# Kernel tuning notes

Hardware: AMD Instinct MI355X
Metric: run time of the kernel (lower is better)

## Reference

```python
import jax, jax.numpy as jnp
import numpy as np

N_IN = 512
SCALE = 0  # s / n_in**scale == s when scale=0

def setup_inputs() -> dict:
    key = jax.random.key(0)
    k1, k2, k3, k4 = jax.random.split(key, 4)
    B, S, D = 4, 128, N_IN
    x = jax.random.normal(k1, (B, S, D), dtype=jnp.float32)
    y = jax.random.normal(k2, (B, S, D), dtype=jnp.float32)
    z = jax.random.normal(k3, (B, S, D), dtype=jnp.float32)
    # weight: (n_out, n_in + bias_x, n_in, n_in + bias_y)
    weight = jax.random.normal(k4, (1, D + 1, D, D + 1), dtype=jnp.float32) * 0.02
    return {"x": x, "y": y, "z": z, "weight": weight}

def reference(x, y, z, weight):
    # append bias-1 column to x and y (bias_x=bias_y=True)
    ones = jnp.ones_like(x[..., :1])
    xb = jnp.concatenate([x, ones], axis=-1)           # [b, s, n_in+1]
    yb = jnp.concatenate([y, jnp.ones_like(y[..., :1])], axis=-1)
    # w = z^T W : [b, o, z, i, j]
    w = jnp.einsum('bzk,oikj->bozij', z, weight)
    # s(x,y,z) = x^T (z^T W) y : [b, o, z, x, y]
    s = jnp.einsum('bxi,bozij,byj->bozxy', xb, w, yb)
    # n_out == 1 -> squeeze channel dim; scale == 0 -> divide by n_in**0 == 1
    return jnp.squeeze(s, axis=1) / (N_IN ** SCALE)
```

## Files before the change

### kernel.cpp

```cpp
#include <hip/hip_runtime.h>
#include <stdint.h>


typedef __attribute__((ext_vector_type(8))) short bf16x8;
typedef __attribute__((ext_vector_type(4))) float f32x4;

__device__ __forceinline__ unsigned short f2bf(float f) {
    unsigned int u = __float_as_uint(f);
    u += 0x7fffu + ((u >> 16) & 1u);
    return (unsigned short)(u >> 16);
}

__device__ __forceinline__ void gload_lds16(const void* g, void* l) {
    __builtin_amdgcn_global_load_lds((const __attribute__((address_space(1))) void*)g,
                                     (__attribute__((address_space(3))) void*)l, 16, 0, 0);
}

__global__ __launch_bounds__(256) void k_cast(const float* __restrict__ x,
    const float* __restrict__ y, const float* __restrict__ z,
    unsigned short* __restrict__ xbf, unsigned short* __restrict__ ybf,
    unsigned short* __restrict__ zbf)
{
    int t = blockIdx.x * 256 + threadIdx.x;
    int arr = t >> 15;
    int off = (t & 32767) * 8;
    const float* src = (arr == 0) ? x : (arr == 1) ? y : z;
    unsigned short* dst = (arr == 0) ? xbf : (arr == 1) ? ybf : zbf;
    float4 a = *(const float4*)(src + off);
    float4 b = *(const float4*)(src + off + 4);
    uint4 o;
    o.x = f2bf(a.x) | ((unsigned)f2bf(a.y) << 16);
    o.y = f2bf(a.z) | ((unsigned)f2bf(a.w) << 16);
    o.z = f2bf(b.x) | ((unsigned)f2bf(b.y) << 16);
    o.w = f2bf(b.z) | ((unsigned)f2bf(b.w) << 16);
    *(uint4*)(dst + off) = o;
}

__global__ __launch_bounds__(256) void k_edge(const float* __restrict__ z,
    const float* __restrict__ w, float* __restrict__ a_arr,
    float* __restrict__ c_arr, float* __restrict__ d_arr)
{
    __shared__ float Zs[64][33];
    __shared__ float Bs[32][65];
    int t = threadIdx.x;
    int mb = blockIdx.x % 17, bzb = blockIdx.x / 17;
    int tr = t >> 4, tc = t & 15;
    float acc[4][4] = {};
    for (int k0 = 0; k0 < 512; k0 += 32) {
        __syncthreads();
        {   int row = t >> 2, ko = (t & 3) * 8;
            const float* p = z + (bzb * 64 + row) * 512 + k0 + ko;
            float4 v0 = ((const float4*)p)[0], v1 = ((const float4*)p)[1];
            Zs[row][ko + 0] = v0.x; Zs[row][ko + 1] = v0.y; Zs[row][ko + 2] = v0.z; Zs[row][ko + 3] = v0.w;
            Zs[row][ko + 4] = v1.x; Zs[row][ko + 5] = v1.y; Zs[row][ko + 6] = v1.z; Zs[row][ko + 7] = v1.w;
        }
        {   int kr = t >> 3, mo = (t & 7) * 8;
            for (int e = 0; e < 8; ++e) {
                int m = mb * 64 + mo + e;
                float v = 0.f;
                int krow = k0 + kr;
                if (m < 512)        v = w[(m * 512 + krow) * 513 + 512];
                else if (m < 1024)  v = w[(262144 + krow) * 513 + (m - 512)];
                else if (m == 1024) v = w[(262144 + krow) * 513 + 512];
                Bs[kr][mo + e] = v;
            }
        }
        __syncthreads();
        for (int kk = 0; kk < 32; ++kk) {
            float zr[4], br[4];
            for (int r = 0; r < 4; ++r) zr[r] = Zs[tr * 4 + r][kk];
            for (int c = 0; c < 4; ++c) br[c] = Bs[kk][tc * 4 + c];
            for (int r = 0; r < 4; ++r)
                for (int c = 0; c < 4; ++c) acc[r][c] += zr[r] * br[c];
        }
    }
    for (int r = 0; r < 4; ++r)
        for (int c = 0; c < 4; ++c) {
            int bz = bzb * 64 + tr * 4 + r;
            int m = mb * 64 + tc * 4 + c;
            if (m < 512)        a_arr[bz * 512 + m] = acc[r][c];
            else if (m < 1024)  c_arr[bz * 512 + (m - 512)] = acc[r][c];
            else if (m == 1024) d_arr[bz] = acc[r][c];
        }
}

__global__ __launch_bounds__(512) void k_uv(const float* __restrict__ xf,
    const float* __restrict__ yf, const float* __restrict__ a_arr,
    const float* __restrict__ c_arr, float* __restrict__ u_arr,
    float* __restrict__ v_arr)
{
    __shared__ float part[512];
    int bz = blockIdx.x;
    int b = bz >> 7;
    int t = threadIdx.x, r = t >> 2, q = t & 3;
    {
        const float* xp = xf + (size_t)(b * 128 + r) * 512;
        const float* ap = a_arr + bz * 512;
        float s = 0.f;
        #pragma unroll 4
        for (int c0 = 0; c0 < 32; ++c0) {
            int col = c0 * 16 + q * 4;
            float4 xv = *(const float4*)(xp + col);
            float4 av = *(const float4*)(ap + col);
            s += xv.x * av.x + xv.y * av.y + xv.z * av.z + xv.w * av.w;
        }
        part[t] = s;
    }
    __syncthreads();
    if (t < 128) u_arr[bz * 128 + t] = part[t*4] + part[t*4+1] + part[t*4+2] + part[t*4+3];
    __syncthreads();
    {
        const float* yp = yf + (size_t)(b * 128 + r) * 512;
        const float* cp = c_arr + bz * 512;
        float s = 0.f;
        #pragma unroll 4
        for (int c0 = 0; c0 < 32; ++c0) {
            int col = c0 * 16 + q * 4;
            float4 yv = *(const float4*)(yp + col);
            float4 cv = *(const float4*)(cp + col);
            s += yv.x * cv.x + yv.y * cv.y + yv.z * cv.z + yv.w * cv.w;
        }
        part[t] = s;
    }
    __syncthreads();
    if (t < 128) v_arr[bz * 128 + t] = part[t*4] + part[t*4+1] + part[t*4+2] + part[t*4+3];
}

__global__ __launch_bounds__(512, 2) void k_gemm1(const unsigned short* __restrict__ zbf,
    const float* __restrict__ w, unsigned short* __restrict__ Mws)
{
    extern __shared__ unsigned char smem[];
    unsigned char* Zb0 = smem;
    unsigned char* Zb1 = smem + 32768;
    unsigned char* Bb0 = smem + 65536;
    unsigned char* Bb1 = smem + 73728;

    int nwg = gridDim.x, cpx = nwg >> 3;
    int bid = blockIdx.x;
    int swz = (bid & 7) * cpx + (bid >> 3);
    int iloc = swz >> 2, jb = swz & 3;
    int j0 = jb * 128;
    int t = threadIdx.x, wid = t >> 6, lane = t & 63;
    int bzg = wid >> 1, jg = wid & 1;
    int l15 = lane & 15, l4 = lane >> 4;

    int arow = lane >> 2;
    int akc  = (lane & 3) ^ ((lane >> 3) & 3);
    const unsigned short* zbase = zbf + (size_t)(wid * 64 + arow) * 512 + akc * 8;

    int jB = t & 127, kq8 = t >> 7;
    const float* wb = w + (size_t)iloc * 262656 + (size_t)(kq8 * 8) * 513 + j0 + jB;
    int bwoff = jB * 64 + ((kq8 ^ ((jB >> 1) & 3)) * 16);

    int aoff = (bzg * 128 + l15) * 64 + ((l4 ^ ((l15 >> 1) & 3)) * 16);
    int boff = (jg * 64 + l15) * 64 + ((l4 ^ ((l15 >> 1) & 3)) * 16);

    f32x4 acc[8][4];
    #pragma unroll
    for (int mt = 0; mt < 8; ++mt)
        #pragma unroll
        for (int nt = 0; nt < 4; ++nt) acc[mt][nt] = (f32x4){0.f, 0.f, 0.f, 0.f};

    float wr[2][8];

    #pragma unroll
    for (int q = 0; q < 4; ++q)
        gload_lds16(zbase + q * 8192, Zb0 + wid * 4096 + q * 1024);
    {
        #pragma unroll
        for (int e = 0; e < 8; ++e) wr[0][e] = __builtin_nontemporal_load(wb + (size_t)e * 513);
        const float* wp = wb + (size_t)32 * 513;
        #pragma unroll
        for (int e = 0; e < 8; ++e) wr[1][e] = __builtin_nontemporal_load(wp + (size_t)e * 513);
        uint4 pk;
        pk.x = f2bf(wr[0][0]) | ((unsigned)f2bf(wr[0][1]) << 16);
        pk.y = f2bf(wr[0][2]) | ((unsigned)f2bf(wr[0][3]) << 16);
        pk.z = f2bf(wr[0][4]) | ((unsigned)f2bf(wr[0][5]) << 16);
        pk.w = f2bf(wr[0][6]) | ((unsigned)f2bf(wr[0][7]) << 16);
        *(uint4*)(Bb0 + bwoff) = pk;
    }
    asm volatile("s_waitcnt lgkmcnt(0)" ::: "memory");
    __builtin_amdgcn_s_barrier();
    __builtin_amdgcn_sched_barrier(0);

    #pragma unroll
    for (int ks = 0; ks < 16; ++ks) {
        const int cur = ks & 1;
        unsigned char* Zcur  = cur ? Zb1 : Zb0;
        unsigned char* Znext = cur ? Zb0 : Zb1;
        unsigned char* Bcur  = cur ? Bb1 : Bb0;
        unsigned char* Bnext = cur ? Bb0 : Bb1;

        if (ks < 15) {
            #pragma unroll
            for (int q = 0; q < 4; ++q)
                gload_lds16(zbase + (ks + 1) * 32 + q * 8192, Znext + wid * 4096 + q * 1024);
        }
        if (ks < 14) {
            const float* wp = wb + (size_t)(ks + 2) * 32 * 513;
            #pragma unroll
            for (int e = 0; e < 8; ++e) wr[cur][e] = __builtin_nontemporal_load(wp + (size_t)e * 513);
        }
        bf16x8 bfr[4];
        #pragma unroll
        for (int nt = 0; nt < 4; ++nt)
            bfr[nt] = *(const bf16x8*)(Bcur + boff + nt * 1024);
        #pragma unroll
        for (int mt = 0; mt < 8; ++mt) {
            bf16x8 afr = *(const bf16x8*)(Zcur + aoff + mt * 1024);
            #pragma unroll
            for (int nt = 0; nt < 4; ++nt)
                acc[mt][nt] = __builtin_amdgcn_mfma_f32_16x16x32_bf16(afr, bfr[nt], acc[mt][nt], 0, 0, 0);
        }
        if (ks < 15) {
            uint4 pk;
            pk.x = f2bf(wr[cur ^ 1][0]) | ((unsigned)f2bf(wr[cur ^ 1][1]) << 16);
            pk.y = f2bf(wr[cur ^ 1][2]) | ((unsigned)f2bf(wr[cur ^ 1][3]) << 16);
            pk.z = f2bf(wr[cur ^ 1][4]) | ((unsigned)f2bf(wr[cur ^ 1][5]) << 16);
            pk.w = f2bf(wr[cur ^ 1][6]) | ((unsigned)f2bf(wr[cur ^ 1][7]) << 16);
            *(uint4*)(Bnext + bwoff) = pk;
        }
        if (ks < 14) {
            asm volatile("s_waitcnt vmcnt(8) lgkmcnt(0)" ::: "memory");
        } else if (ks == 14) {
            asm volatile("s_waitcnt vmcnt(0) lgkmcnt(0)" ::: "memory");
        }
        if (ks < 15) {
            __builtin_amdgcn_s_barrier();
            __builtin_amdgcn_sched_barrier(0);
        }
    }

    #pragma unroll
    for (int mt = 0; mt < 8; ++mt)
        #pragma unroll
        for (int nt = 0; nt < 4; ++nt)
            #pragma unroll
            for (int r = 0; r < 4; ++r) {
                int bz = bzg * 128 + mt * 16 + l4 * 4 + r;
                int j  = j0 + jg * 64 + nt * 16 + l15;
                Mws[(size_t)bz * 262144 + (size_t)iloc * 512 + j] = f2bf(acc[mt][nt][r]);
            }
}

__global__ __launch_bounds__(512, 2) void k_fuse(const unsigned short* __restrict__ xbf,
    const unsigned short* __restrict__ ybf, const unsigned short* __restrict__ Mws,
    const float* __restrict__ u_arr, const float* __restrict__ v_arr,
    const float* __restrict__ d_arr, float* __restrict__ out)
{
    extern __shared__ unsigned char smem[];

    int bid = blockIdx.x;
    int bz = (bid & 7) * 64 + (bid >> 3);
    int b = bz >> 7;
    int t = threadIdx.x, wid = t >> 6, lane = t & 63;
    int l15 = lane & 15, l4 = lane >> 4;
    int xg = wid >> 2, yg = wid & 3;
    int g8 = wid;

    const unsigned short* ybase = ybf + (size_t)(b * 128) * 512;
    #pragma unroll
    for (int it = 0; it < 16; ++it) {
        int row = it * 8 + wid;
        gload_lds16(ybase + (size_t)row * 512 + ((lane ^ (row & 63)) * 8),
                    smem + it * 8192 + t * 16);
    }

    const unsigned short* mbase = Mws + (size_t)bz * 262144
                                + (size_t)(g8 * 64 + l15) * 512 + l4 * 8;
    bf16x8 mfr[4][4];
    #pragma unroll
    for (int d = 0; d < 4; ++d)
        #pragma unroll
        for (int mt = 0; mt < 4; ++mt)
            mfr[d][mt] = *(const bf16x8*)(mbase + (size_t)mt * 8192 + d * 32);

    asm volatile("s_waitcnt vmcnt(16)" ::: "memory");
    __builtin_amdgcn_s_barrier();
    __builtin_amdgcn_sched_barrier(0);

    f32x4 accR[4][8];
    #pragma unroll
    for (int mt = 0; mt < 4; ++mt)
        #pragma unroll
        for (int nt = 0; nt < 8; ++nt) accR[mt][nt] = (f32x4){0.f, 0.f, 0.f, 0.f};

    #pragma unroll
    for (int kf = 0; kf < 16; ++kf) {
        #pragma unroll
        for (int nh = 0; nh < 2; ++nh) {
            bf16x8 yfr[4];
            #pragma unroll
            for (int n4 = 0; n4 < 4; ++n4) {
                int y = (nh * 4 + n4) * 16 + l15;
                yfr[n4] = *(const bf16x8*)(smem + y * 1024 + (((kf * 4 + l4) ^ (y & 63)) * 16));
            }
            #pragma unroll
            for (int mt = 0; mt < 4; ++mt)
                #pragma unroll
                for (int n4 = 0; n4 < 4; ++n4)
                    accR[mt][nh * 4 + n4] = __builtin_amdgcn_mfma_f32_16x16x32_bf16(
                        mfr[kf & 3][mt], yfr[n4], accR[mt][nh * 4 + n4], 0, 0, 0);
        }
        if (kf < 12) {
            #pragma unroll
            for (int mt = 0; mt < 4; ++mt)
                mfr[kf & 3][mt] = *(const bf16x8*)(mbase + (size_t)mt * 8192 + (kf + 4) * 32);
        }
    }

    const unsigned short* xbase = xbf + (size_t)(b * 128 + xg * 64 + l15) * 512 + l4 * 8;
    bf16x8 xfr[3][4];
    #pragma unroll
    for (int d = 0; d < 3; ++d)
        #pragma unroll
        for (int mt = 0; mt < 4; ++mt)
            xfr[d][mt] = *(const bf16x8*)(xbase + (size_t)mt * 8192 + d * 32);

    asm volatile("s_waitcnt lgkmcnt(0)" ::: "memory");
    __builtin_amdgcn_s_barrier();
    __builtin_amdgcn_sched_barrier(0);

    #pragma unroll
    for (int mt = 0; mt < 4; ++mt)
        #pragma unroll
        for (int nt = 0; nt < 8; ++nt) {
            int y = nt * 16 + l15;
            int chunk = g8 * 8 + mt * 2 + (l4 >> 1);
            int byte = y * 1024 + ((chunk ^ (y & 63)) * 16) + (l4 & 1) * 8;
            unsigned p0 = f2bf(accR[mt][nt][0]) | ((unsigned)f2bf(accR[mt][nt][1]) << 16);
            unsigned p1 = f2bf(accR[mt][nt][2]) | ((unsigned)f2bf(accR[mt][nt][3]) << 16);
            *(uint2*)(smem + byte) = make_uint2(p0, p1);
        }
    asm volatile("s_waitcnt lgkmcnt(0)" ::: "memory");
    __builtin_amdgcn_s_barrier();
    __builtin_amdgcn_sched_barrier(0);

    f32x4 acc[4][2];
    #pragma unroll
    for (int mt = 0; mt < 4; ++mt)
        #pragma unroll
        for (int nt = 0; nt < 2; ++nt) acc[mt][nt] = (f32x4){0.f, 0.f, 0.f, 0.f};

    #pragma unroll
    for (int kf = 0; kf < 16; ++kf) {
        bf16x8 rfr[2];
        #pragma unroll
        for (int nt = 0; nt < 2; ++nt) {
            int y = yg * 32 + nt * 16 + l15;
            rfr[nt] = *(const bf16x8*)(smem + y * 1024 + (((kf * 4 + l4) ^ (y & 63)) * 16));
        }
        #pragma unroll
        for (int mt = 0; mt < 4; ++mt)
            #pragma unroll
            for (int nt = 0; nt < 2; ++nt)
                acc[mt][nt] = __builtin_amdgcn_mfma_f32_16x16x32_bf16(
                    xfr[kf % 3][mt], rfr[nt], acc[mt][nt], 0, 0, 0);
        if (kf < 13) {
            #pragma unroll
            for (int mt = 0; mt < 4; ++mt)
                xfr[kf % 3][mt] = *(const bf16x8*)(xbase + (size_t)mt * 8192 + (kf + 3) * 32);
        }
    }

    float dv = d_arr[bz];
    float* op = out + (size_t)bz * 16384;
    #pragma unroll
    for (int mt = 0; mt < 4; ++mt) {
        float4 uq = *(const float4*)(u_arr + bz * 128 + xg * 64 + mt * 16 + l4 * 4);
        #pragma unroll
        for (int nt = 0; nt < 2; ++nt) {
            int y = yg * 32 + nt * 16 + l15;
            float vv = v_arr[bz * 128 + y] + dv;
            int x0 = xg * 64 + mt * 16 + l4 * 4;
            op[(x0 + 0) * 128 + y] = acc[mt][nt][0] + uq.x + vv;
            op[(x0 + 1) * 128 + y] = acc[mt][nt][1] + uq.y + vv;
            op[(x0 + 2) * 128 + y] = acc[mt][nt][2] + uq.z + vv;
            op[(x0 + 3) * 128 + y] = acc[mt][nt][3] + uq.w + vv;
        }
    }
}

extern "C" void kernel_launch(void* const* d_in, const int* in_sizes, int n_in,
                              void* d_out, int out_size, void* d_ws, size_t ws_size,
                              hipStream_t stream)
{
    const float* x = (const float*)d_in[0];
    const float* y = (const float*)d_in[1];
    const float* z = (const float*)d_in[2];
    const float* w = (const float*)d_in[3];
    float* out = (float*)d_out;
    char* ws = (char*)d_ws;

    unsigned short* xbf = (unsigned short*)(ws + 0);
    unsigned short* ybf = (unsigned short*)(ws + 524288);
    unsigned short* zbf = (unsigned short*)(ws + 1048576);
    float* a_arr = (float*)(ws + 1572864);
    float* c_arr = (float*)(ws + 2621440);
    float* d_arr = (float*)(ws + 3670016);
    float* u_arr = (float*)(ws + 3674112);
    float* v_arr = (float*)(ws + 3936256);
    unsigned short* Mws = (unsigned short*)(ws + 4198400);

    hipLaunchKernelGGL(k_cast, dim3(384), dim3(256), 0, stream, x, y, z, xbf, ybf, zbf);
    hipLaunchKernelGGL(k_edge, dim3(136), dim3(256), 0, stream, z, w, a_arr, c_arr, d_arr);
    hipLaunchKernelGGL(k_uv, dim3(512), dim3(512), 0, stream, x, y, a_arr, c_arr, u_arr, v_arr);
    hipLaunchKernelGGL(k_gemm1, dim3(2048), dim3(512), 81920, stream, zbf, w, Mws);
    hipLaunchKernelGGL(k_fuse, dim3(512), dim3(512), 131072, stream, xbf, ybf, Mws,
                       u_arr, v_arr, d_arr, out);
}
```

Measured before the change: 445.5 us.

## Retile gemm1 to 256x256 tiles with K=64 stages and phased MFMA schedule

Restructures the z×W GEMM kernel from 512x128 output tiles with K=32 steps to 256x256 tiles with K=64 steps, each split into four barrier-separated MFMA phases. The aim is less per-iteration barrier and fp32-to-bf16 weight-conversion overhead per MFMA, better reuse of each loaded weight column, and overlap of global loads with compute through an interleaved ping-pong schedule and s_setprio. The cost is 128KB of LDS per block, which likely limits each CU to one block, plus more barriers per K-step and plain rather than nontemporal weight loads.

```diff
diff --git a/kernel.cpp b/kernel.cpp
--- a/kernel.cpp
+++ b/kernel.cpp
@@ -130,116 +130,153 @@
     const float* __restrict__ w, unsigned short* __restrict__ Mws)
 {
     extern __shared__ unsigned char smem[];
-    unsigned char* Zb0 = smem;
-    unsigned char* Zb1 = smem + 32768;
-    unsigned char* Bb0 = smem + 65536;
-    unsigned char* Bb1 = smem + 73728;
-
-    int nwg = gridDim.x, cpx = nwg >> 3;
+    unsigned char* const Ab0 = smem;
+    unsigned char* const Ab1 = smem + 32768;
+    unsigned char* const Bb0 = smem + 65536;
+    unsigned char* const Bb1 = smem + 98304;
+
     int bid = blockIdx.x;
-    int swz = (bid & 7) * cpx + (bid >> 3);
-    int iloc = swz >> 2, jb = swz & 3;
-    int j0 = jb * 128;
+    int swz = (bid & 7) * 256 + (bid >> 3);
+    int mt2 = swz & 1;
+    int panel = swz >> 1;
+    int jb = panel & 1, iw = panel >> 1;
+    int bz0 = mt2 * 256;
+    int jlo = jb * 256;
     int t = threadIdx.x, wid = t >> 6, lane = t & 63;
-    int bzg = wid >> 1, jg = wid & 1;
+    int wm = wid >> 2, wn = wid & 3;
     int l15 = lane & 15, l4 = lane >> 4;
 
-    int arow = lane >> 2;
-    int akc  = (lane & 3) ^ ((lane >> 3) & 3);
-    const unsigned short* zbase = zbf + (size_t)(wid * 64 + arow) * 512 + akc * 8;
-
-    int jB = t & 127, kq8 = t >> 7;
-    const float* wb = w + (size_t)iloc * 262656 + (size_t)(kq8 * 8) * 513 + j0 + jB;
-    int bwoff = jB * 64 + ((kq8 ^ ((jB >> 1) & 3)) * 16);
-
-    int aoff = (bzg * 128 + l15) * 64 + ((l4 ^ ((l15 >> 1) & 3)) * 16);
-    int boff = (jg * 64 + l15) * 64 + ((l4 ^ ((l15 >> 1) & 3)) * 16);
+    int ar = t >> 3;
+    int ac = (t & 7) ^ (ar & 7);
+    const unsigned short* zsrc = zbf + (size_t)(bz0 + ar) * 512 + ac * 8;
+
+    int jB = t & 127, s2 = t >> 7;
+    const float* wsrc = w + (size_t)iw * 262656 + (size_t)(s2 * 16) * 513 + jlo + jB;
+    int bw0 = jB * 128 + (((s2 * 2)     ^ (jB & 7)) * 16);
+    int bw1 = jB * 128 + (((s2 * 2 + 1) ^ (jB & 7)) * 16);
+
+    int axr = l15 & 7;
+    int abase = (wm * 128 + l15) * 128;
+    int bbase = (wn * 64 + l15) * 128;
 
     f32x4 acc[8][4];
     #pragma unroll
-    for (int mt = 0; mt < 8; ++mt)
-        #pragma unroll
-        for (int nt = 0; nt < 4; ++nt) acc[mt][nt] = (f32x4){0.f, 0.f, 0.f, 0.f};
-
-    float wr[2][8];
-
-    #pragma unroll
-    for (int q = 0; q < 4; ++q)
-        gload_lds16(zbase + q * 8192, Zb0 + wid * 4096 + q * 1024);
-    {
-        #pragma unroll
-        for (int e = 0; e < 8; ++e) wr[0][e] = __builtin_nontemporal_load(wb + (size_t)e * 513);
-        const float* wp = wb + (size_t)32 * 513;
-        #pragma unroll
-        for (int e = 0; e < 8; ++e) wr[1][e] = __builtin_nontemporal_load(wp + (size_t)e * 513);
-        uint4 pk;
-        pk.x = f2bf(wr[0][0]) | ((unsigned)f2bf(wr[0][1]) << 16);
-        pk.y = f2bf(wr[0][2]) | ((unsigned)f2bf(wr[0][3]) << 16);
-        pk.z = f2bf(wr[0][4]) | ((unsigned)f2bf(wr[0][5]) << 16);
-        pk.w = f2bf(wr[0][6]) | ((unsigned)f2bf(wr[0][7]) << 16);
-        *(uint4*)(Bb0 + bwoff) = pk;
-    }
-    asm volatile("s_waitcnt lgkmcnt(0)" ::: "memory");
+    for (int f = 0; f < 8; ++f)
+        #pragma unroll
+        for (int g = 0; g < 4; ++g) acc[f][g] = (f32x4){0.f, 0.f, 0.f, 0.f};
+
+    float wr0[16], wr1[16];
+    bf16x8 af[4][2], bfA[2][2], bfB[2][2];
+
+#define LDW(dst, kt, h) { const float* _p = wsrc + (size_t)(kt) * 64 * 513 + (h) * 128; \
+    _Pragma("unroll") for (int _e = 0; _e < 16; ++_e) dst[_e] = _p[(size_t)_e * 513]; }
+
+#define STAGE_A(buf, kt) { int _ko = (kt) * 64; \
+    gload_lds16(zsrc + _ko,          (buf) + t * 16); \
+    gload_lds16(zsrc + 32768 + _ko,  (buf) + 8192 + t * 16); \
+    gload_lds16(zsrc + 65536 + _ko,  (buf) + 16384 + t * 16); \
+    gload_lds16(zsrc + 98304 + _ko,  (buf) + 24576 + t * 16); }
+
+#define PACKW(buf, half, src) { uint4 _pa, _pb; \
+    _pa.x = f2bf(src[0])  | ((unsigned)f2bf(src[1])  << 16); \
+    _pa.y = f2bf(src[2])  | ((unsigned)f2bf(src[3])  << 16); \
+    _pa.z = f2bf(src[4])  | ((unsigned)f2bf(src[5])  << 16); \
+    _pa.w = f2bf(src[6])  | ((unsigned)f2bf(src[7])  << 16); \
+    _pb.x = f2bf(src[8])  | ((unsigned)f2bf(src[9])  << 16); \
+    _pb.y = f2bf(src[10]) | ((unsigned)f2bf(src[11]) << 16); \
+    _pb.z = f2bf(src[12]) | ((unsigned)f2bf(src[13]) << 16); \
+    _pb.w = f2bf(src[14]) | ((unsigned)f2bf(src[15]) << 16); \
+    *(uint4*)((buf) + (half) * 16384 + bw0) = _pa; \
+    *(uint4*)((buf) + (half) * 16384 + bw1) = _pb; }
+
+#define LD_A(buf, mq) { _Pragma("unroll") for (int _f = 0; _f < 4; ++_f) \
+    _Pragma("unroll") for (int _kc = 0; _kc < 2; ++_kc) \
+    af[_f][_kc] = *(const bf16x8*)((buf) + abase + ((mq) * 64 + _f * 16) * 128 \
+                                   + (((_kc * 4 + l4) ^ axr) * 16)); }
+
+#define LD_B(buf, nq, dst) { _Pragma("unroll") for (int _g = 0; _g < 2; ++_g) \
+    _Pragma("unroll") for (int _kc = 0; _kc < 2; ++_kc) \
+    dst[_g][_kc] = *(const bf16x8*)((buf) + bbase + ((nq) * 32 + _g * 16) * 128 \
+                                    + (((_kc * 4 + l4) ^ axr) * 16)); }
+
+#define MM(mq, nq, bfr) { _Pragma("unroll") for (int _f = 0; _f < 4; ++_f) \
+    _Pragma("unroll") for (int _g = 0; _g < 2; ++_g) \
+    _Pragma("unroll") for (int _kc = 0; _kc < 2; ++_kc) \
+    acc[(mq) * 4 + _f][(nq) * 2 + _g] = __builtin_amdgcn_mfma_f32_16x16x32_bf16( \
+        af[_f][_kc], bfr[_g][_kc], acc[(mq) * 4 + _f][(nq) * 2 + _g], 0, 0, 0); }
+
+#define PH_SYNC() { __builtin_amdgcn_s_barrier(); \
+    asm volatile("s_waitcnt lgkmcnt(0)" ::: "memory"); \
+    __builtin_amdgcn_sched_barrier(0); }
+#define PH_END() { __builtin_amdgcn_s_barrier(); __builtin_amdgcn_sched_barrier(0); }
+
+    LDW(wr0, 0, 0);
+    LDW(wr1, 0, 1);
+    STAGE_A(Ab0, 0);
+    PACKW(Bb0, 0, wr0);
+    PACKW(Bb0, 1, wr1);
+    asm volatile("s_waitcnt vmcnt(0) lgkmcnt(0)" ::: "memory");
     __builtin_amdgcn_s_barrier();
     __builtin_amdgcn_sched_barrier(0);
 
     #pragma unroll
-    for (int ks = 0; ks < 16; ++ks) {
-        const int cur = ks & 1;
-        unsigned char* Zcur  = cur ? Zb1 : Zb0;
-        unsigned char* Znext = cur ? Zb0 : Zb1;
-        unsigned char* Bcur  = cur ? Bb1 : Bb0;
-        unsigned char* Bnext = cur ? Bb0 : Bb1;
-
-        if (ks < 15) {
-            #pragma unroll
-            for (int q = 0; q < 4; ++q)
-                gload_lds16(zbase + (ks + 1) * 32 + q * 8192, Znext + wid * 4096 + q * 1024);
-        }
-        if (ks < 14) {
-            const float* wp = wb + (size_t)(ks + 2) * 32 * 513;
-            #pragma unroll
-            for (int e = 0; e < 8; ++e) wr[cur][e] = __builtin_nontemporal_load(wp + (size_t)e * 513);
-        }
-        bf16x8 bfr[4];
-        #pragma unroll
-        for (int nt = 0; nt < 4; ++nt)
-            bfr[nt] = *(const bf16x8*)(Bcur + boff + nt * 1024);
-        #pragma unroll
-        for (int mt = 0; mt < 8; ++mt) {
-            bf16x8 afr = *(const bf16x8*)(Zcur + aoff + mt * 1024);
-            #pragma unroll
-            for (int nt = 0; nt < 4; ++nt)
-                acc[mt][nt] = __builtin_amdgcn_mfma_f32_16x16x32_bf16(afr, bfr[nt], acc[mt][nt], 0, 0, 0);
-        }
-        if (ks < 15) {
-            uint4 pk;
-            pk.x = f2bf(wr[cur ^ 1][0]) | ((unsigned)f2bf(wr[cur ^ 1][1]) << 16);
-            pk.y = f2bf(wr[cur ^ 1][2]) | ((unsigned)f2bf(wr[cur ^ 1][3]) << 16);
-            pk.z = f2bf(wr[cur ^ 1][4]) | ((unsigned)f2bf(wr[cur ^ 1][5]) << 16);
-            pk.w = f2bf(wr[cur ^ 1][6]) | ((unsigned)f2bf(wr[cur ^ 1][7]) << 16);
-            *(uint4*)(Bnext + bwoff) = pk;
-        }
-        if (ks < 14) {
-            asm volatile("s_waitcnt vmcnt(8) lgkmcnt(0)" ::: "memory");
-        } else if (ks == 14) {
-            asm volatile("s_waitcnt vmcnt(0) lgkmcnt(0)" ::: "memory");
-        }
-        if (ks < 15) {
-            __builtin_amdgcn_s_barrier();
-            __builtin_amdgcn_sched_barrier(0);
-        }
-    }
-
-    #pragma unroll
-    for (int mt = 0; mt < 8; ++mt)
-        #pragma unroll
-        for (int nt = 0; nt < 4; ++nt)
+    for (int kt = 0; kt < 8; ++kt) {
+        unsigned char* Ac = (kt & 1) ? Ab1 : Ab0;
+        unsigned char* Bc = (kt & 1) ? Bb1 : Bb0;
+        unsigned char* An = (kt & 1) ? Ab0 : Ab1;
+        unsigned char* Bn = (kt & 1) ? Bb0 : Bb1;
+
+        LD_A(Ac, 0);
+        LD_B(Bc, 0, bfA);
+        if (kt < 7) { LDW(wr0, kt + 1, 0); STAGE_A(An, kt + 1); }
+        PH_SYNC();
+        __builtin_amdgcn_s_setprio(1);
+        MM(0, 0, bfA);
+        __builtin_amdgcn_s_setprio(0);
+        PH_END();
+
+        LD_B(Bc, 1, bfB);
+        if (kt < 7) { LDW(wr1, kt + 1, 1); }
+        PH_SYNC();
+        __builtin_amdgcn_s_setprio(1);
+        MM(0, 1, bfB);
+        __builtin_amdgcn_s_setprio(0);
+        PH_END();
+
+        LD_A(Ac, 1);
+        if (kt < 7) { PACKW(Bn, 0, wr0); }
+        PH_SYNC();
+        __builtin_amdgcn_s_setprio(1);
+        MM(1, 0, bfA);
+        __builtin_amdgcn_s_setprio(0);
+        PH_END();
+
+        if (kt < 7) { PACKW(Bn, 1, wr1); }
+        PH_SYNC();
+        __builtin_amdgcn_s_setprio(1);
+        MM(1, 1, bfB);
+        __builtin_amdgcn_s_setprio(0);
+        if (kt < 7) PH_END();
+    }
+
+#undef LDW
+#undef STAGE_A
+#undef PACKW
+#undef LD_A
+#undef LD_B
+#undef MM
+#undef PH_SYNC
+#undef PH_END
+
+    #pragma unroll
+    for (int f = 0; f < 8; ++f)
+        #pragma unroll
+        for (int g = 0; g < 4; ++g)
             #pragma unroll
             for (int r = 0; r < 4; ++r) {
-                int bz = bzg * 128 + mt * 16 + l4 * 4 + r;
-                int j  = j0 + jg * 64 + nt * 16 + l15;
-                Mws[(size_t)bz * 262144 + (size_t)iloc * 512 + j] = f2bf(acc[mt][nt][r]);
+                int bz = bz0 + wm * 128 + f * 16 + l4 * 4 + r;
+                int jg = jlo + wn * 64 + g * 16 + l15;
+                Mws[(size_t)bz * 262144 + (size_t)iw * 512 + jg] = f2bf(acc[f][g][r]);
             }
 }
 
@@ -405,7 +442,7 @@
     hipLaunchKernelGGL(k_cast, dim3(384), dim3(256), 0, stream, x, y, z, xbf, ybf, zbf);
     hipLaunchKernelGGL(k_edge, dim3(136), dim3(256), 0, stream, z, w, a_arr, c_arr, d_arr);
     hipLaunchKernelGGL(k_uv, dim3(512), dim3(512), 0, stream, x, y, a_arr, c_arr, u_arr, v_arr);
-    hipLaunchKernelGGL(k_gemm1, dim3(2048), dim3(512), 81920, stream, zbf, w, Mws);
+    hipLaunchKernelGGL(k_gemm1, dim3(2048), dim3(512), 131072, stream, zbf, w, Mws);
     hipLaunchKernelGGL(k_fuse, dim3(512), dim3(512), 131072, stream, xbf, ybf, Mws,
                        u_arr, v_arr, d_arr, out);
 }
```

Result: slower. 574.7 us (+29.0%).

## Stage fp32 weights directly into LDS via async loads and convert at fragment read

Applied to the files above, without the earlier changes.

The gemm1 kernel's weight operand used to be loaded into registers as fp32, converted to bf16 and stored to LDS, with loads issued two stages ahead. Now raw fp32 weight tiles are copied straight to LDS using global_load_lds with an XOR swizzle, and the bf16 conversion moves to the point where the B fragments are read, using scalar LDS reads. The goal is to free VGPRs and VALU work in the global-to-LDS path and make the weight copy asynchronous. The cost is double the LDS footprint for B (98KB per block, which may hurt the two-blocks-per-CU occupancy), 32 scalar LDS reads per step instead of four vector reads, repeated conversion work across waves, and a shallower prefetch with a full vmcnt(0) wait each iteration.

```diff
diff --git a/kernel.cpp b/kernel.cpp
--- a/kernel.cpp
+++ b/kernel.cpp
@@ -133,7 +133,7 @@
     unsigned char* Zb0 = smem;
     unsigned char* Zb1 = smem + 32768;
     unsigned char* Bb0 = smem + 65536;
-    unsigned char* Bb1 = smem + 73728;
+    unsigned char* Bb1 = smem + 81920;
 
     int nwg = gridDim.x, cpx = nwg >> 3;
     int bid = blockIdx.x;
@@ -147,13 +147,25 @@
     int arow = lane >> 2;
     int akc  = (lane & 3) ^ ((lane >> 3) & 3);
     const unsigned short* zbase = zbf + (size_t)(wid * 64 + arow) * 512 + akc * 8;
-
-    int jB = t & 127, kq8 = t >> 7;
-    const float* wb = w + (size_t)iloc * 262656 + (size_t)(kq8 * 8) * 513 + j0 + jB;
-    int bwoff = jB * 64 + ((kq8 ^ ((jB >> 1) & 3)) * 16);
-
     int aoff = (bzg * 128 + l15) * 64 + ((l4 ^ ((l15 >> 1) & 3)) * 16);
-    int boff = (jg * 64 + l15) * 64 + ((l4 ^ ((l15 >> 1) & 3)) * 16);
+
+    const float* wbase = w + (size_t)iloc * 262656 + j0;
+    int kofs[2], jofs[2];
+    #pragma unroll
+    for (int g = 0; g < 2; ++g) {
+        int idx = g * 64 + lane;
+        int k_t = wid * 4 + (idx >> 5);
+        int q = idx & 31;
+        int q_src = q ^ (((k_t >> 3) & 3) << 2);
+        kofs[g] = k_t;
+        jofs[g] = q_src * 4;
+    }
+    int bjq[4];
+    #pragma unroll
+    for (int nt = 0; nt < 4; ++nt) {
+        int j = jg * 64 + nt * 16 + l15;
+        bjq[nt] = (((j >> 2) ^ (l4 << 2)) * 16) + ((j & 3) * 4) + (l4 * 8) * 512;
+    }
 
     f32x4 acc[8][4];
     #pragma unroll
@@ -161,25 +173,17 @@
         #pragma unroll
         for (int nt = 0; nt < 4; ++nt) acc[mt][nt] = (f32x4){0.f, 0.f, 0.f, 0.f};
 
-    float wr[2][8];
-
-    #pragma unroll
-    for (int q = 0; q < 4; ++q)
-        gload_lds16(zbase + q * 8192, Zb0 + wid * 4096 + q * 1024);
-    {
-        #pragma unroll
-        for (int e = 0; e < 8; ++e) wr[0][e] = __builtin_nontemporal_load(wb + (size_t)e * 513);
-        const float* wp = wb + (size_t)32 * 513;
-        #pragma unroll
-        for (int e = 0; e < 8; ++e) wr[1][e] = __builtin_nontemporal_load(wp + (size_t)e * 513);
-        uint4 pk;
-        pk.x = f2bf(wr[0][0]) | ((unsigned)f2bf(wr[0][1]) << 16);
-        pk.y = f2bf(wr[0][2]) | ((unsigned)f2bf(wr[0][3]) << 16);
-        pk.z = f2bf(wr[0][4]) | ((unsigned)f2bf(wr[0][5]) << 16);
-        pk.w = f2bf(wr[0][6]) | ((unsigned)f2bf(wr[0][7]) << 16);
-        *(uint4*)(Bb0 + bwoff) = pk;
-    }
-    asm volatile("s_waitcnt lgkmcnt(0)" ::: "memory");
+#define STAGE_A(buf, ks1) { \
+    _Pragma("unroll") for (int q = 0; q < 4; ++q) \
+        gload_lds16(zbase + (ks1) * 32 + q * 8192, (buf) + wid * 4096 + q * 1024); }
+#define STAGE_B(buf, ks1) { \
+    _Pragma("unroll") for (int g = 0; g < 2; ++g) \
+        gload_lds16(wbase + (size_t)((ks1) * 32 + kofs[g]) * 513 + jofs[g], \
+                    (buf) + wid * 2048 + g * 1024); }
+
+    STAGE_A(Zb0, 0);
+    STAGE_B(Bb0, 0);
+    asm volatile("s_waitcnt vmcnt(0)" ::: "memory");
     __builtin_amdgcn_s_barrier();
     __builtin_amdgcn_sched_barrier(0);
 
@@ -192,19 +196,23 @@
         unsigned char* Bnext = cur ? Bb0 : Bb1;
 
         if (ks < 15) {
-            #pragma unroll
-            for (int q = 0; q < 4; ++q)
-                gload_lds16(zbase + (ks + 1) * 32 + q * 8192, Znext + wid * 4096 + q * 1024);
-        }
-        if (ks < 14) {
-            const float* wp = wb + (size_t)(ks + 2) * 32 * 513;
-            #pragma unroll
-            for (int e = 0; e < 8; ++e) wr[cur][e] = __builtin_nontemporal_load(wp + (size_t)e * 513);
+            STAGE_A(Znext, ks + 1);
+            STAGE_B(Bnext, ks + 1);
         }
         bf16x8 bfr[4];
         #pragma unroll
-        for (int nt = 0; nt < 4; ++nt)
-            bfr[nt] = *(const bf16x8*)(Bcur + boff + nt * 1024);
+        for (int nt = 0; nt < 4; ++nt) {
+            float bfv[8];
+            #pragma unroll
+            for (int e = 0; e < 8; ++e)
+                bfv[e] = *(const float*)(Bcur + bjq[nt] + e * 512);
+            union { unsigned u[4]; bf16x8 v; } pk;
+            pk.u[0] = f2bf(bfv[0]) | ((unsigned)f2bf(bfv[1]) << 16);
+            pk.u[1] = f2bf(bfv[2]) | ((unsigned)f2bf(bfv[3]) << 16);
+            pk.u[2] = f2bf(bfv[4]) | ((unsigned)f2bf(bfv[5]) << 16);
+            pk.u[3] = f2bf(bfv[6]) | ((unsigned)f2bf(bfv[7]) << 16);
+            bfr[nt] = pk.v;
+        }
         #pragma unroll
         for (int mt = 0; mt < 8; ++mt) {
             bf16x8 afr = *(const bf16x8*)(Zcur + aoff + mt * 1024);
@@ -213,23 +221,13 @@
                 acc[mt][nt] = __builtin_amdgcn_mfma_f32_16x16x32_bf16(afr, bfr[nt], acc[mt][nt], 0, 0, 0);
         }
         if (ks < 15) {
-            uint4 pk;
-            pk.x = f2bf(wr[cur ^ 1][0]) | ((unsigned)f2bf(wr[cur ^ 1][1]) << 16);
-            pk.y = f2bf(wr[cur ^ 1][2]) | ((unsigned)f2bf(wr[cur ^ 1][3]) << 16);
-            pk.z = f2bf(wr[cur ^ 1][4]) | ((unsigned)f2bf(wr[cur ^ 1][5]) << 16);
-            pk.w = f2bf(wr[cur ^ 1][6]) | ((unsigned)f2bf(wr[cur ^ 1][7]) << 16);
-            *(uint4*)(Bnext + bwoff) = pk;
-        }
-        if (ks < 14) {
-            asm volatile("s_waitcnt vmcnt(8) lgkmcnt(0)" ::: "memory");
-        } else if (ks == 14) {
             asm volatile("s_waitcnt vmcnt(0) lgkmcnt(0)" ::: "memory");
-        }
-        if (ks < 15) {
             __builtin_amdgcn_s_barrier();
             __builtin_amdgcn_sched_barrier(0);
         }
     }
+#undef STAGE_A
+#undef STAGE_B
 
     #pragma unroll
     for (int mt = 0; mt < 8; ++mt)
@@ -405,7 +403,7 @@
     hipLaunchKernelGGL(k_cast, dim3(384), dim3(256), 0, stream, x, y, z, xbf, ybf, zbf);
     hipLaunchKernelGGL(k_edge, dim3(136), dim3(256), 0, stream, z, w, a_arr, c_arr, d_arr);
     hipLaunchKernelGGL(k_uv, dim3(512), dim3(512), 0, stream, x, y, a_arr, c_arr, u_arr, v_arr);
-    hipLaunchKernelGGL(k_gemm1, dim3(2048), dim3(512), 81920, stream, zbf, w, Mws);
+    hipLaunchKernelGGL(k_gemm1, dim3(2048), dim3(512), 98304, stream, zbf, w, Mws);
     hipLaunchKernelGGL(k_fuse, dim3(512), dim3(512), 131072, stream, xbf, ybf, Mws,
                        u_arr, v_arr, d_arr, out);
 }
```

Measured after the change: 511.6 us. +14.9%, slower.
